# Performance work log

Hardware: AMD Instinct MI355X
Metric: run time of the kernel (lower is better)

The kernel has to match this reference:

```python
import jax, jax.numpy as jnp
import numpy as np

TOPK = 12
D = 256
SCALE = D ** -0.5


def setup_inputs() -> dict:
    key = jax.random.key(0)
    ks = jax.random.split(key, 6)
    N, D_in = 12288, 1024
    def w(k, shape, fan_in):
        return jax.random.normal(k, shape, jnp.float32) / np.float32(np.sqrt(fan_in))
    return {
        "x_path": jax.random.normal(ks[0], (N, D_in), jnp.float32),
        "wsi_w": w(ks[1], (D_in, D), D_in),
        "wsi_b": jnp.zeros((D,), jnp.float32),
        "wh_w": w(ks[2], (D, D), D),
        "wh_b": jnp.zeros((D,), jnp.float32),
        "wt_w": w(ks[3], (D, D), D),
        "wt_b": jnp.zeros((D,), jnp.float32),
        "w1_w": w(ks[4], (D, D), D),
        "w1_b": jnp.zeros((D,), jnp.float32),
        "w2_w": w(ks[5], (D, D), D),
        "w2_b": jnp.zeros((D,), jnp.float32),
    }


def reference(x_path, wsi_w, wsi_b, wh_w, wh_b, wt_w, wt_b, w1_w, w1_b, w2_w, w2_b):
    # wsi_net: Linear(1024,256) + ReLU (dropout is identity in eval)
    h = jax.nn.relu(x_path @ wsi_w + wsi_b)          # [N, D]
    e_h = h @ wh_w + wh_b                            # [N, D]
    e_t = h @ wt_w + wt_b                            # [N, D]
    # dense scaled similarity: [N, N]
    attn_logit = (e_h * SCALE) @ e_t.T
    topk_weight, topk_index = jax.lax.top_k(attn_logit, TOPK)  # [N, K]
    topk_prob = jax.nn.softmax(topk_weight, axis=-1)           # [N, K]
    # gather top-k neighbor tail embeddings
    Nb_h = e_t[topk_index]                           # [N, K, D]
    # eh_r = p * Nb_h + (1-p) (x) e_h   (outer product == broadcast mul)
    eh_r = topk_prob[..., None] * Nb_h + (1.0 - topk_prob)[..., None] * e_h[:, None, :]
    gate = jnp.tanh(e_h[:, None, :] + eh_r)          # [N, K, D]
    ka_weight = jnp.einsum('nkd,nkd->nk', Nb_h, gate)  # [N, K]
    ka_prob = jax.nn.softmax(ka_weight, axis=-1)       # [N, K]
    e_Nh = jnp.einsum('nk,nkd->nd', ka_prob, Nb_h)     # [N, D]
    sum_embedding = jax.nn.relu((e_h + e_Nh) @ w1_w + w1_b)
    bi_embedding = jax.nn.relu((e_h * e_Nh) @ w2_w + w2_b)
    return sum_embedding + bi_embedding              # [N, D]
```

## Files before the change

kernel.cpp:

```cpp
#include <hip/hip_runtime.h>
#include <hip/hip_bf16.h>
#include <cmath>

#define TK 12
#define NROW 12288
#define NEG_BIG (-3.0e38f)
#define MFMA16(a,b,c) __builtin_amdgcn_mfma_f32_16x16x32_f16(a,b,c,0,0,0)

#define NCH 8
#define CTILES 96
#define NPH 48
#define NGRP_TOT 384
#define CAP 256

typedef _Float16 f16x8 __attribute__((ext_vector_type(8)));
typedef _Float16 f16x4 __attribute__((ext_vector_type(4)));
typedef float    f32x4 __attribute__((ext_vector_type(4)));

typedef __attribute__((address_space(1))) const void gvoid_t;
typedef __attribute__((address_space(3))) void lvoid_t;
__device__ __forceinline__ void gload_lds16(const void* g, void* l) {
    __builtin_amdgcn_global_load_lds((gvoid_t*)g, (lvoid_t*)l, 16, 0, 0);
}

__global__ __launch_bounds__(256) void wpack(
    const float* __restrict__ W, _Float16* __restrict__ hi,
    _Float16* __restrict__ lo, int N, int nkt)
{
    const int tid = blockIdx.x * 256 + threadIdx.x;
    const int l = tid & 63;
    const int s = (tid >> 6) % nkt;
    const int cg = tid / (nkt * 64);
    const int krow = s * 32 + 8 * (l >> 4);
    const int col = cg * 16 + (l & 15);
    f16x8 H, L;
    #pragma unroll
    for (int j = 0; j < 8; ++j) {
        float w = W[(size_t)(krow + j) * N + col];
        _Float16 h = (_Float16)w;
        H[j] = h;
        L[j] = (_Float16)(w - (float)h);
    }
    *(f16x8*)(hi + (size_t)tid * 8) = H;
    *(f16x8*)(lo + (size_t)tid * 8) = L;
}

__global__ __launch_bounds__(256) void wpack4(
    const float* __restrict__ W0, const float* __restrict__ W1,
    const float* __restrict__ W2, const float* __restrict__ W3,
    _Float16* __restrict__ base)
{
    const int m = blockIdx.y;
    const float* W = (m == 0) ? W0 : (m == 1) ? W1 : (m == 2) ? W2 : W3;
    _Float16* hi = base + (size_t)m * 131072;
    _Float16* lo = hi + 65536;
    const int tid = blockIdx.x * 256 + threadIdx.x;
    const int l = tid & 63;
    const int s = (tid >> 6) & 7;
    const int cg = tid >> 9;
    const int krow = s * 32 + 8 * (l >> 4);
    const int col = cg * 16 + (l & 15);
    f16x8 H, L;
    #pragma unroll
    for (int j = 0; j < 8; ++j) {
        float w = W[(size_t)(krow + j) * 256 + col];
        _Float16 h = (_Float16)w;
        H[j] = h;
        L[j] = (_Float16)(w - (float)h);
    }
    *(f16x8*)(hi + (size_t)tid * 8) = H;
    *(f16x8*)(lo + (size_t)tid * 8) = L;
}

template<bool RELU>
__global__ __launch_bounds__(256) void gemm_mfma(
    const float* __restrict__ A1,
    const _Float16* __restrict__ Wh, const _Float16* __restrict__ Wl,
    const float* __restrict__ bias, float* __restrict__ C, int K)
{
    __shared__ _Float16 aH[2048], aL[2048];
    __shared__ _Float16 wH[2048], wL[2048];
    const int tid = threadIdx.x, lane = tid & 63, wave = tid >> 6;
    const int rb = blockIdx.y * 64;
    const int cbg = blockIdx.x * 4;
    const int nkt = K >> 5;

    const int arow = rb + wave * 16 + (lane & 15);
    const int acol0 = 8 * (lane >> 4);
    const float* a1p = A1 + (size_t)arow * K + acol0;
    const size_t wbase = ((size_t)(cbg + wave) * nkt) * 512 + lane * 8;

    f32x4 acc[4];
    #pragma unroll
    for (int rg = 0; rg < 4; ++rg) acc[rg] = (f32x4){0.f,0.f,0.f,0.f};

    float4 pa0 = *(const float4*)(a1p);
    float4 pa1 = *(const float4*)(a1p + 4);
    f16x8 pwh = *(const f16x8*)(Wh + wbase);
    f16x8 pwl = *(const f16x8*)(Wl + wbase);

    for (int kt = 0; kt < nkt; ++kt) {
        __syncthreads();
        {
            float v[8] = {pa0.x, pa0.y, pa0.z, pa0.w, pa1.x, pa1.y, pa1.z, pa1.w};
            f16x8 H, L;
            #pragma unroll
            for (int j = 0; j < 8; ++j) {
                _Float16 h = (_Float16)v[j];
                H[j] = h;
                L[j] = (_Float16)(v[j] - (float)h);
            }
            *(f16x8*)&aH[tid*8] = H;
            *(f16x8*)&aL[tid*8] = L;
            *(f16x8*)&wH[tid*8] = pwh;
            *(f16x8*)&wL[tid*8] = pwl;
        }
        __syncthreads();
        if (kt + 1 < nkt) {
            pa0 = *(const float4*)(a1p + (kt+1)*32);
            pa1 = *(const float4*)(a1p + (kt+1)*32 + 4);
            pwh = *(const f16x8*)(Wh + wbase + (size_t)(kt+1)*512);
            pwl = *(const f16x8*)(Wl + wbase + (size_t)(kt+1)*512);
        }
        f16x8 wh = *(const f16x8*)&wH[(wave*64 + lane)*8];
        f16x8 wl = *(const f16x8*)&wL[(wave*64 + lane)*8];
        #pragma unroll
        for (int rg = 0; rg < 4; ++rg) {
            f16x8 ah = *(const f16x8*)&aH[(rg*64 + lane)*8];
            f16x8 al = *(const f16x8*)&aL[(rg*64 + lane)*8];
            acc[rg] = MFMA16(wh, ah, acc[rg]);
            acc[rg] = MFMA16(wl, ah, acc[rg]);
            acc[rg] = MFMA16(wh, al, acc[rg]);
        }
    }
    const int col = (cbg + wave)*16 + 4*(lane >> 4);
    float4 b4 = *(const float4*)(bias + col);
    #pragma unroll
    for (int rg = 0; rg < 4; ++rg) {
        const int row = rb + rg*16 + (lane & 15);
        float4 o;
        o.x = acc[rg][0] + b4.x; o.y = acc[rg][1] + b4.y;
        o.z = acc[rg][2] + b4.z; o.w = acc[rg][3] + b4.w;
        if (RELU) {
            o.x = fmaxf(o.x, 0.f); o.y = fmaxf(o.y, 0.f);
            o.z = fmaxf(o.z, 0.f); o.w = fmaxf(o.w, 0.f);
        }
        *(float4*)(C + (size_t)row*256 + col) = o;
    }
}

template<int DMODE>
__global__ __launch_bounds__(256) void gemm_dual(
    const float* __restrict__ A1, const float* __restrict__ A2,
    const _Float16* __restrict__ W1h, const _Float16* __restrict__ W1l,
    const _Float16* __restrict__ W2h, const _Float16* __restrict__ W2l,
    const float* __restrict__ bias1, const float* __restrict__ bias2,
    float* __restrict__ C1, float* __restrict__ C2,
    _Float16* __restrict__ P1, _Float16* __restrict__ P2)
{
    __shared__ _Float16 aH[2][2048], aL[2][2048];
    __shared__ _Float16 wH[2][2048], wL[2][2048];
    const int tid = threadIdx.x, lane = tid & 63, wave = tid >> 6;
    const int rb = blockIdx.y * 64;
    const int cbg = blockIdx.x * 4;

    const int arow = rb + wave * 16 + (lane & 15);
    const int acol0 = 8 * (lane >> 4);
    const float* a1p = A1 + (size_t)arow * 256 + acol0;
    const float* a2p = (DMODE == 1) ? (A2 + (size_t)arow * 256 + acol0) : nullptr;
    const size_t wbase = ((size_t)(cbg + wave) * 8) * 512 + lane * 8;

    f32x4 acc1[4], acc2[4];
    #pragma unroll
    for (int rg = 0; rg < 4; ++rg) {
        acc1[rg] = (f32x4){0.f,0.f,0.f,0.f};
        acc2[rg] = (f32x4){0.f,0.f,0.f,0.f};
    }

    float4 pa0 = *(const float4*)(a1p);
    float4 pa1 = *(const float4*)(a1p + 4);
    float4 pb0, pb1;
    if (DMODE == 1) { pb0 = *(const float4*)(a2p); pb1 = *(const float4*)(a2p + 4); }
    f16x8 pw1h = *(const f16x8*)(W1h + wbase);
    f16x8 pw1l = *(const f16x8*)(W1l + wbase);
    f16x8 pw2h = *(const f16x8*)(W2h + wbase);
    f16x8 pw2l = *(const f16x8*)(W2l + wbase);

    for (int kt = 0; kt < 8; ++kt) {
        __syncthreads();
        {
            float v[8] = {pa0.x, pa0.y, pa0.z, pa0.w, pa1.x, pa1.y, pa1.z, pa1.w};
            if (DMODE == 0) {
                f16x8 H, L;
                #pragma unroll
                for (int j = 0; j < 8; ++j) {
                    _Float16 h = (_Float16)v[j];
                    H[j] = h;
                    L[j] = (_Float16)(v[j] - (float)h);
                }
                *(f16x8*)&aH[0][tid*8] = H;
                *(f16x8*)&aL[0][tid*8] = L;
            } else {
                float b[8] = {pb0.x, pb0.y, pb0.z, pb0.w, pb1.x, pb1.y, pb1.z, pb1.w};
                f16x8 Hs, Ls, Hm, Lm;
                #pragma unroll
                for (int j = 0; j < 8; ++j) {
                    float s = v[j] + b[j];
                    float m = v[j] * b[j];
                    _Float16 hs = (_Float16)s;
                    _Float16 hm = (_Float16)m;
                    Hs[j] = hs; Ls[j] = (_Float16)(s - (float)hs);
                    Hm[j] = hm; Lm[j] = (_Float16)(m - (float)hm);
                }
                *(f16x8*)&aH[0][tid*8] = Hs;
                *(f16x8*)&aL[0][tid*8] = Ls;
                *(f16x8*)&aH[1][tid*8] = Hm;
                *(f16x8*)&aL[1][tid*8] = Lm;
            }
            *(f16x8*)&wH[0][tid*8] = pw1h;
            *(f16x8*)&wL[0][tid*8] = pw1l;
            *(f16x8*)&wH[1][tid*8] = pw2h;
            *(f16x8*)&wL[1][tid*8] = pw2l;
        }
        __syncthreads();
        if (kt + 1 < 8) {
            pa0 = *(const float4*)(a1p + (kt+1)*32);
            pa1 = *(const float4*)(a1p + (kt+1)*32 + 4);
            if (DMODE == 1) {
                pb0 = *(const float4*)(a2p + (kt+1)*32);
                pb1 = *(const float4*)(a2p + (kt+1)*32 + 4);
            }
            pw1h = *(const f16x8*)(W1h + wbase + (size_t)(kt+1)*512);
            pw1l = *(const f16x8*)(W1l + wbase + (size_t)(kt+1)*512);
            pw2h = *(const f16x8*)(W2h + wbase + (size_t)(kt+1)*512);
            pw2l = *(const f16x8*)(W2l + wbase + (size_t)(kt+1)*512);
        }
        f16x8 w1h = *(const f16x8*)&wH[0][(wave*64 + lane)*8];
        f16x8 w1l = *(const f16x8*)&wL[0][(wave*64 + lane)*8];
        f16x8 w2h = *(const f16x8*)&wH[1][(wave*64 + lane)*8];
        f16x8 w2l = *(const f16x8*)&wL[1][(wave*64 + lane)*8];
        #pragma unroll
        for (int rg = 0; rg < 4; ++rg) {
            f16x8 ah0 = *(const f16x8*)&aH[0][(rg*64 + lane)*8];
            f16x8 al0 = *(const f16x8*)&aL[0][(rg*64 + lane)*8];
            acc1[rg] = MFMA16(w1h, ah0, acc1[rg]);
            acc1[rg] = MFMA16(w1l, ah0, acc1[rg]);
            acc1[rg] = MFMA16(w1h, al0, acc1[rg]);
            f16x8 ah1 = (DMODE == 1) ? *(const f16x8*)&aH[1][(rg*64 + lane)*8] : ah0;
            f16x8 al1 = (DMODE == 1) ? *(const f16x8*)&aL[1][(rg*64 + lane)*8] : al0;
            acc2[rg] = MFMA16(w2h, ah1, acc2[rg]);
            acc2[rg] = MFMA16(w2l, ah1, acc2[rg]);
            acc2[rg] = MFMA16(w2h, al1, acc2[rg]);
        }
    }
    const int col = (cbg + wave)*16 + 4*(lane >> 4);
    float4 b14 = *(const float4*)(bias1 + col);
    float4 b24 = *(const float4*)(bias2 + col);
    #pragma unroll
    for (int rg = 0; rg < 4; ++rg) {
        const int row = rb + rg*16 + (lane & 15);
        if (DMODE == 0) {
            float4 o1, o2;
            o1.x = acc1[rg][0] + b14.x; o1.y = acc1[rg][1] + b14.y;
            o1.z = acc1[rg][2] + b14.z; o1.w = acc1[rg][3] + b14.w;
            o2.x = acc2[rg][0] + b24.x; o2.y = acc2[rg][1] + b24.y;
            o2.z = acc2[rg][2] + b24.z; o2.w = acc2[rg][3] + b24.w;
            *(float4*)(C1 + (size_t)row*256 + col) = o1;
            *(float4*)(C2 + (size_t)row*256 + col) = o2;
            const size_t poff = ((size_t)(row >> 4)*8 + (col >> 5))*512
                              + (((col & 31) >> 3)*16 + (row & 15))*8 + (col & 7);
            f16x4 p1, p2;
            p1[0] = (_Float16)(o1.x * 0.0625f); p1[1] = (_Float16)(o1.y * 0.0625f);
            p1[2] = (_Float16)(o1.z * 0.0625f); p1[3] = (_Float16)(o1.w * 0.0625f);
            p2[0] = (_Float16)o2.x; p2[1] = (_Float16)o2.y;
            p2[2] = (_Float16)o2.z; p2[3] = (_Float16)o2.w;
            *(f16x4*)(P1 + poff) = p1;
            *(f16x4*)(P2 + poff) = p2;
        } else {
            float4 o;
            o.x = fmaxf(acc1[rg][0] + b14.x, 0.f) + fmaxf(acc2[rg][0] + b24.x, 0.f);
            o.y = fmaxf(acc1[rg][1] + b14.y, 0.f) + fmaxf(acc2[rg][1] + b24.y, 0.f);
            o.z = fmaxf(acc1[rg][2] + b14.z, 0.f) + fmaxf(acc2[rg][2] + b24.z, 0.f);
            o.w = fmaxf(acc1[rg][3] + b14.w, 0.f) + fmaxf(acc2[rg][3] + b24.w, 0.f);
            *(float4*)(C1 + (size_t)row*256 + col) = o;
        }
    }
}

__global__ __launch_bounds__(256, 2) void s1_gmax(
    const _Float16* __restrict__ ehh, const _Float16* __restrict__ eth,
    unsigned* __restrict__ g32, unsigned char* __restrict__ gcol)
{
    __shared__ _Float16 abuf[3][8192];
    const int tid = threadIdx.x, lane = tid & 63, wave = tid >> 6;
    const int chunk = blockIdx.x & (NCH-1);
    const int rblk = blockIdx.x >> 3;
    const int rg0 = rblk * 8 + wave * 2;

    f16x8 bh[2][8];
    #pragma unroll
    for (int rs = 0; rs < 2; ++rs) {
        const _Float16* p = ehh + (size_t)(rg0 + rs)*4096 + lane*8;
        #pragma unroll
        for (int s = 0; s < 8; ++s) bh[rs][s] = *(const f16x8*)(p + s*512);
    }
    #pragma unroll
    for (int rs = 0; rs < 2; ++rs)
        #pragma unroll
        for (int s = 0; s < 8; ++s)
            asm volatile("" : "+v"(bh[rs][s]));

    const int rsw = (lane >> 4) & 1;
    const int myrow = (rg0 + rsw)*16 + (lane & 15);
    const size_t rowbase = (size_t)myrow*NGRP_TOT + chunk*NPH;

    const _Float16* gsrc = eth + (size_t)chunk * CTILES * 4096;
    #pragma unroll
    for (int ph = 0; ph < 2; ++ph) {
        #pragma unroll
        for (int i = 0; i < 4; ++i) {
            const int u = wave*4 + i;
            gload_lds16(gsrc + (size_t)(ph*2 + (u>>3))*4096 + (u&7)*512 + lane*8,
                        &abuf[ph][u*512]);
        }
    }
    asm volatile("s_waitcnt vmcnt(4) lgkmcnt(0)" ::: "memory");
    __builtin_amdgcn_s_barrier();
    asm volatile("" ::: "memory");

    int cur = 0;
    for (int pp = 0; pp < 6; ++pp) {
        unsigned resv[8];
        unsigned long long colv = 0;
        #pragma unroll
        for (int q = 0; q < 8; ++q) {
            const int p = pp*8 + q;
            int nx = cur + 2; if (nx >= 3) nx -= 3;
            if (p + 2 < NPH) {
                #pragma unroll
                for (int i = 0; i < 4; ++i) {
                    const int u = wave*4 + i;
                    gload_lds16(gsrc + (size_t)((p+2)*2 + (u>>3))*4096 + (u&7)*512 + lane*8,
                                &abuf[nx][u*512]);
                }
            }
            float m1a = NEG_BIG, m2a = NEG_BIG; int mca = 0;
            float m1b = NEG_BIG, m2b = NEG_BIG; int mcb = 0;
            __builtin_amdgcn_s_setprio(1);
            #pragma unroll
            for (int tt = 0; tt < 2; ++tt) {
                f32x4 aE[2], aO[2];
                #pragma unroll
                for (int rs = 0; rs < 2; ++rs) {
                    aE[rs] = (f32x4){0.f,0.f,0.f,0.f};
                    aO[rs] = (f32x4){0.f,0.f,0.f,0.f};
                }
                #pragma unroll
                for (int s = 0; s < 8; ++s) {
                    f16x8 ah = *(const f16x8*)&abuf[cur][tt*4096 + s*512 + lane*8];
                    if (s & 1) {
                        aO[0] = MFMA16(ah, bh[0][s], aO[0]);
                        aO[1] = MFMA16(ah, bh[1][s], aO[1]);
                    } else {
                        aE[0] = MFMA16(ah, bh[0][s], aE[0]);
                        aE[1] = MFMA16(ah, bh[1][s], aE[1]);
                    }
                }
                f32x4 a0 = aE[0] + aO[0];
                f32x4 a1 = aE[1] + aO[1];
                const int cb = tt*16 + 4*(lane >> 4);
                #pragma unroll
                for (int e = 0; e < 4; ++e) {
                    bool g0 = a0[e] > m1a;
                    m2a = fmaxf(m2a, g0 ? m1a : a0[e]);
                    mca = g0 ? (cb + e) : mca;
                    m1a = fmaxf(m1a, a0[e]);
                    bool g1 = a1[e] > m1b;
                    m2b = fmaxf(m2b, g1 ? m1b : a1[e]);
                    mcb = g1 ? (cb + e) : mcb;
                    m1b = fmaxf(m1b, a1[e]);
                }
            }
            __builtin_amdgcn_s_setprio(0);
            #pragma unroll
            for (int k = 16; k <= 32; k <<= 1) {
                float o1 = __shfl_xor(m1a, k); int oc = __shfl_xor(mca, k);
                float o2 = __shfl_xor(m2a, k);
                bool gt = o1 > m1a;
                m2a = fmaxf(fmaxf(m2a, o2), gt ? m1a : o1);
                mca = gt ? oc : mca;
                m1a = fmaxf(m1a, o1);
                float p1 = __shfl_xor(m1b, k); int pc = __shfl_xor(mcb, k);
                float p2 = __shfl_xor(m2b, k);
                bool ht = p1 > m1b;
                m2b = fmaxf(fmaxf(m2b, p2), ht ? m1b : p1);
                mcb = ht ? pc : mcb;
                m1b = fmaxf(m1b, p1);
            }
            {
                float M1 = rsw ? m1b : m1a;
                float M2 = rsw ? m2b : m2a;
                int   MC = rsw ? mcb : mca;
                unsigned short h1 = __builtin_bit_cast(unsigned short, (_Float16)M1);
                unsigned short h2 = __builtin_bit_cast(unsigned short, (_Float16)M2);
                resv[q] = ((unsigned)h1 << 16) | h2;
                colv |= (unsigned long long)(unsigned char)MC << (8*q);
            }
            if (q == 7 && lane < 32) {
                const size_t base = rowbase + pp*8;
                uint4 v0; v0.x = resv[0]; v0.y = resv[1]; v0.z = resv[2]; v0.w = resv[3];
                uint4 v1; v1.x = resv[4]; v1.y = resv[5]; v1.z = resv[6]; v1.w = resv[7];
                *(uint4*)(g32 + base)     = v0;
                *(uint4*)(g32 + base + 4) = v1;
                *(unsigned long long*)(gcol + base) = colv;
            }
            if (p + 2 < NPH) {
                if (q == 7) { asm volatile("s_waitcnt vmcnt(7)" ::: "memory"); }
                else        { asm volatile("s_waitcnt vmcnt(4)" ::: "memory"); }
            } else {
                asm volatile("s_waitcnt vmcnt(0)" ::: "memory");
            }
            __builtin_amdgcn_s_barrier();
            asm volatile("" ::: "memory");
            cur = cur + 1; if (cur >= 3) cur = 0;
        }
    }
    asm volatile("s_waitcnt vmcnt(0)" ::: "memory");
}

__global__ __launch_bounds__(256) void b2_emit(
    const unsigned* __restrict__ g32, const unsigned char* __restrict__ gcol,
    unsigned* __restrict__ cnt, int* __restrict__ cand)
{
    const int lane = threadIdx.x & 63;
    const int wave = threadIdx.x >> 6;
    const int row  = blockIdx.x * 4 + wave;

    const unsigned* gr = g32 + (size_t)row*NGRP_TOT + lane*6;
    uint2 u0 = *(const uint2*)gr;
    uint2 u1 = *(const uint2*)(gr + 2);
    uint2 u2 = *(const uint2*)(gr + 4);
    unsigned uu[6] = {u0.x, u0.y, u1.x, u1.y, u2.x, u2.y};
    float m1[6], m2[6];
    #pragma unroll
    for (int i = 0; i < 6; ++i) {
        m1[i] = (float)__builtin_bit_cast(_Float16, (unsigned short)(uu[i] >> 16));
        m2[i] = (float)__builtin_bit_cast(_Float16, (unsigned short)(uu[i] & 0xffffu));
    }

    float sl[6];
    #pragma unroll
    for (int j = 0; j < 6; ++j) sl[j] = NEG_BIG;
    #pragma unroll
    for (int i = 0; i < 6; ++i) {
        float v = m1[i];
        #pragma unroll
        for (int j = 5; j >= 1; --j)
            sl[j] = __builtin_amdgcn_fmed3f(v, sl[j], sl[j-1]);
        sl[0] = fmaxf(v, sl[0]);
    }

    int hi = 0;
    float t12 = NEG_BIG;
    #pragma unroll 1
    for (int o = 0; o < TK; ++o) {
        float head = (hi < 6) ? sl[hi] : NEG_BIG;
        float bv = head; int bl = lane;
        #pragma unroll
        for (int off = 1; off <= 32; off <<= 1) {
            float ov = __shfl_xor(bv, off);
            int   ol = __shfl_xor(bl, off);
            bool take = (ov > bv) || (ov == bv && ol < bl);
            bv = take ? ov : bv;
            bl = take ? ol : bl;
        }
        if (lane == bl) hi++;
        t12 = bv;
    }
    const float tau = t12 - 0.02f;

    int n = 0;
    int* crow = cand + (size_t)row * CAP;
    #pragma unroll 1
    for (int i = 0; i < 6; ++i) {
        const bool hit1 = m1[i] >= tau;
        const bool expn = hit1 && (m2[i] >= tau);
        const bool single = hit1 && !expn;
        unsigned long long ms = __ballot(single);
        if (single) {
            const int pos = n + __popcll(ms & ((1ull << lane) - 1ull));
            if (pos < CAP) {
                const int g = lane*6 + i;
                crow[pos] = g*32 + (int)gcol[(size_t)row*NGRP_TOT + g];
            }
        }
        n += __popcll(ms);
        unsigned long long me = __ballot(expn);
        while (me) {
            const int src = __builtin_ctzll(me);
            me &= me - 1ull;
            const int cb = (src*6 + i) * 32;
            if (lane < 32) {
                const int pos = n + lane;
                if (pos < CAP) crow[pos] = cb + lane;
            }
            n += 32;
        }
    }
    if (lane == 0) cnt[row] = (unsigned)((n < CAP) ? n : CAP);
}

__global__ __launch_bounds__(256) void s3_tail(
    const float* __restrict__ e_h, const float* __restrict__ e_t,
    const unsigned int* __restrict__ cnt, const int* __restrict__ cand,
    float* __restrict__ e_Nh)
{
    __shared__ float sbuf[4][64];
    const int lane = threadIdx.x & 63;
    const int wave = threadIdx.x >> 6;
    const int row  = blockIdx.x * 4 + wave;
    const int quad = lane & 3;
    const int cg   = lane >> 2;

    const int cn = (int)min(cnt[row], (unsigned)CAP);
    const float* ehr = e_h + (size_t)row * 256;

    float4 ehv[16];
    #pragma unroll
    for (int j = 0; j < 16; ++j)
        ehv[j] = *(const float4*)(ehr + j*16 + quad*4);

    float v[4]; int c[4];
    #pragma unroll
    for (int i = 0; i < 4; ++i) {
        const int idx = lane + 64*i;
        c[i] = (idx < cn) ? cand[(size_t)row*CAP + idx] : (0x7ffffff0 + i);
        v[i] = NEG_BIG;
    }

    #pragma unroll 1
    for (int ch = 0; ch < 4; ++ch) {
        if (cn <= 64*ch) break;
        #pragma unroll
        for (int b = 0; b < 4; ++b) {
            const int ci = ch*64 + b*16 + cg;
            const bool act = ci < cn;
            const int col = act ? cand[(size_t)row*CAP + ci] : 0;
            const float* etr = e_t + (size_t)col * 256;
            float s = 0.f;
            #pragma unroll
            for (int j = 0; j < 16; ++j) {
                float4 bb = *(const float4*)(etr + j*16 + quad*4);
                s += ehv[j].x*bb.x + ehv[j].y*bb.y + ehv[j].z*bb.z + ehv[j].w*bb.w;
            }
            s += __shfl_xor(s, 1);
            s += __shfl_xor(s, 2);
            if (quad == 0) sbuf[wave][b*16 + cg] = s;
        }
        const int idx = ch*64 + lane;
        float sv = sbuf[wave][lane];
        if (idx < cn) v[ch] = sv * 0.0625f;
    }

    float tvv[TK]; int ti[TK];
    #pragma unroll
    for (int o = 0; o < TK; ++o) {
        float bv = v[0]; int bc = c[0];
        #pragma unroll
        for (int i = 1; i < 4; ++i) {
            bool take = (v[i] > bv) || (v[i] == bv && c[i] < bc);
            bv = take ? v[i] : bv;
            bc = take ? c[i] : bc;
        }
        #pragma unroll
        for (int off = 32; off; off >>= 1) {
            float ov = __shfl_xor(bv, off);
            int   oc = __shfl_xor(bc, off);
            bool take = (ov > bv) || (ov == bv && oc < bc);
            bv = take ? ov : bv;
            bc = take ? oc : bc;
        }
        tvv[o] = bv; ti[o] = bc;
        #pragma unroll
        for (int i = 0; i < 4; ++i)
            if (c[i] == bc) v[i] = NEG_BIG;
    }

    float p[TK]; float Z = 0.f;
    #pragma unroll
    for (int j = 0; j < TK; ++j) { p[j] = expf(tvv[j] - tvv[0]); Z += p[j]; }
    const float invZ = 1.f / Z;
    #pragma unroll
    for (int j = 0; j < TK; ++j) p[j] *= invZ;

    float4 eh = *(const float4*)(ehr + lane * 4);

    float4 nb[TK]; float kw[TK];
    #pragma unroll
    for (int k = 0; k < TK; ++k) {
        float4 n = *(const float4*)(e_t + (size_t)ti[k] * 256 + lane * 4);
        nb[k] = n;
        const float pk = p[k], qk = 1.f - p[k];
        float4 gt;
        gt.x = tanhf(eh.x + (pk * n.x + qk * eh.x));
        gt.y = tanhf(eh.y + (pk * n.y + qk * eh.y));
        gt.z = tanhf(eh.z + (pk * n.z + qk * eh.z));
        gt.w = tanhf(eh.w + (pk * n.w + qk * eh.w));
        float d = n.x*gt.x + n.y*gt.y + n.z*gt.z + n.w*gt.w;
        #pragma unroll
        for (int off = 32; off; off >>= 1) d += __shfl_xor(d, off);
        kw[k] = d;
    }

    float km = kw[0];
    #pragma unroll
    for (int k = 1; k < TK; ++k) km = fmaxf(km, kw[k]);
    float kz = 0.f; float kp[TK];
    #pragma unroll
    for (int k = 0; k < TK; ++k) { kp[k] = expf(kw[k] - km); kz += kp[k]; }
    const float invKZ = 1.f / kz;

    float4 acc = make_float4(0.f, 0.f, 0.f, 0.f);
    #pragma unroll
    for (int k = 0; k < TK; ++k) {
        acc.x += kp[k] * nb[k].x;
        acc.y += kp[k] * nb[k].y;
        acc.z += kp[k] * nb[k].z;
        acc.w += kp[k] * nb[k].w;
    }
    acc.x *= invKZ; acc.y *= invKZ; acc.z *= invKZ; acc.w *= invKZ;
    *(float4*)(e_Nh + (size_t)row * 256 + lane * 4) = acc;
}

extern "C" void kernel_launch(void* const* d_in, const int* in_sizes, int n_in,
                              void* d_out, int out_size, void* d_ws, size_t ws_size,
                              hipStream_t stream)
{
    (void)in_sizes; (void)n_in; (void)out_size; (void)ws_size;
    const float* x     = (const float*)d_in[0];
    const float* wsi_w = (const float*)d_in[1];
    const float* wsi_b = (const float*)d_in[2];
    const float* wh_w  = (const float*)d_in[3];
    const float* wh_b  = (const float*)d_in[4];
    const float* wt_w  = (const float*)d_in[5];
    const float* wt_b  = (const float*)d_in[6];
    const float* w1_w  = (const float*)d_in[7];
    const float* w1_b  = (const float*)d_in[8];
    const float* w2_w  = (const float*)d_in[9];
    const float* w2_b  = (const float*)d_in[10];
    float* out = (float*)d_out;
    float* ws  = (float*)d_ws;

    const int M = NROW;
    const size_t ND = (size_t)M * 256;

    float* h    = ws;
    float* e_h  = ws + ND;
    float* e_t  = ws + 2*ND;
    _Float16* ehh = (_Float16*)(ws + 3*ND);
    _Float16* eth = (_Float16*)(ws + 3*ND + ND/2);
    size_t o = 4*ND;
    unsigned* g32 = (unsigned*)(ws + o);          o += (size_t)NGRP_TOT*NROW;
    unsigned char* gcol = (unsigned char*)(ws + o); o += (size_t)NGRP_TOT*NROW/4;
    unsigned int* cnt = (unsigned int*)(ws + o);  o += NROW;
    int* cand = (int*)(ws + o);                   o += (size_t)NROW*CAP;
    _Float16* hp = (_Float16*)(ws + o);
    _Float16* wsiH = hp;
    _Float16* wsiL = hp + 262144;
    _Float16* w4base = hp + 524288;
    _Float16* whH  = w4base;
    _Float16* whL  = w4base + 65536;
    _Float16* wtH  = w4base + 2*65536;
    _Float16* wtL  = w4base + 3*65536;
    _Float16* w1H  = w4base + 4*65536;
    _Float16* w1L  = w4base + 5*65536;
    _Float16* w2H  = w4base + 6*65536;
    _Float16* w2L  = w4base + 7*65536;
    float* e_Nh = h;

    wpack<<<128, 256, 0, stream>>>(wsi_w, wsiH, wsiL, 256, 32);
    wpack4<<<dim3(32, 4), 256, 0, stream>>>(wh_w, wt_w, w1_w, w2_w, w4base);

    gemm_mfma<true><<<dim3(4, M/64), 256, 0, stream>>>(
        x, wsiH, wsiL, wsi_b, h, 1024);
    gemm_dual<0><<<dim3(4, M/64), 256, 0, stream>>>(
        h, nullptr, whH, whL, wtH, wtL, wh_b, wt_b, e_h, e_t, ehh, eth);
    s1_gmax<<<NCH*96, 256, 0, stream>>>(ehh, eth, g32, gcol);
    b2_emit<<<M/4, 256, 0, stream>>>(g32, gcol, cnt, cand);
    s3_tail<<<M/4, 256, 0, stream>>>(e_h, e_t, cnt, cand, e_Nh);
    gemm_dual<1><<<dim3(4, M/64), 256, 0, stream>>>(
        e_h, e_Nh, w1H, w1L, w2H, w2L, w1_b, w2_b, out, nullptr, nullptr, nullptr);
}
```

Before: 343.8 us.

## Track top-3 per column group to cut full-group candidate expansion; use fast tanh/exp

The similarity pre-pass now keeps the top three values and two column indices per 32-column group instead of top two and one index. The emit stage can then add up to two exact candidates per group and only expands the whole group when the third value passes the threshold. This is meant to shrink the candidate lists and the rescoring work in the tail kernel, at the price of more compare/select work and twice the per-group summary traffic. Separately, the tail kernel swaps tanhf/expf/division for fast approximate intrinsics, which slightly reduces accuracy.

```diff
diff --git a/kernel.cpp b/kernel.cpp
--- a/kernel.cpp
+++ b/kernel.cpp
@@ -21,6 +21,11 @@
 typedef __attribute__((address_space(3))) void lvoid_t;
 __device__ __forceinline__ void gload_lds16(const void* g, void* l) {
     __builtin_amdgcn_global_load_lds((gvoid_t*)g, (lvoid_t*)l, 16, 0, 0);
+}
+
+__device__ __forceinline__ float ftanh(float x) {
+    float e = __expf(2.f * x);
+    return 1.f - __fdividef(2.f, e + 1.f);
 }
 
 __global__ __launch_bounds__(256) void wpack(
@@ -287,9 +292,17 @@
     }
 }
 
+#define INS3(v, c, M1, C1v, M2, C2v, M3)                 \
+    { bool g1 = (v) > M1, g2 = (v) > M2, g3 = (v) > M3;  \
+      M3 = g2 ? M2 : (g3 ? (v) : M3);                    \
+      M2 = g1 ? M1 : (g2 ? (v) : M2);                    \
+      C2v = g1 ? C1v : (g2 ? (c) : C2v);                 \
+      M1 = g1 ? (v) : M1;                                \
+      C1v = g1 ? (c) : C1v; }
+
 __global__ __launch_bounds__(256, 2) void s1_gmax(
     const _Float16* __restrict__ ehh, const _Float16* __restrict__ eth,
-    unsigned* __restrict__ g32, unsigned char* __restrict__ gcol)
+    uint2* __restrict__ g64)
 {
     __shared__ _Float16 abuf[3][8192];
     const int tid = threadIdx.x, lane = tid & 63, wave = tid >> 6;
@@ -330,8 +343,7 @@
 
     int cur = 0;
     for (int pp = 0; pp < 6; ++pp) {
-        unsigned resv[8];
-        unsigned long long colv = 0;
+        unsigned resx[8], resy[8];
         #pragma unroll
         for (int q = 0; q < 8; ++q) {
             const int p = pp*8 + q;
@@ -344,8 +356,8 @@
                                 &abuf[nx][u*512]);
                 }
             }
-            float m1a = NEG_BIG, m2a = NEG_BIG; int mca = 0;
-            float m1b = NEG_BIG, m2b = NEG_BIG; int mcb = 0;
+            float m1a = NEG_BIG, m2a = NEG_BIG, m3a = NEG_BIG; int c1a = 0, c2a = 0;
+            float m1b = NEG_BIG, m2b = NEG_BIG, m3b = NEG_BIG; int c1b = 0, c2b = 0;
             __builtin_amdgcn_s_setprio(1);
             #pragma unroll
             for (int tt = 0; tt < 2; ++tt) {
@@ -371,51 +383,51 @@
                 const int cb = tt*16 + 4*(lane >> 4);
                 #pragma unroll
                 for (int e = 0; e < 4; ++e) {
-                    bool g0 = a0[e] > m1a;
-                    m2a = fmaxf(m2a, g0 ? m1a : a0[e]);
-                    mca = g0 ? (cb + e) : mca;
-                    m1a = fmaxf(m1a, a0[e]);
-                    bool g1 = a1[e] > m1b;
-                    m2b = fmaxf(m2b, g1 ? m1b : a1[e]);
-                    mcb = g1 ? (cb + e) : mcb;
-                    m1b = fmaxf(m1b, a1[e]);
+                    INS3(a0[e], cb + e, m1a, c1a, m2a, c2a, m3a);
+                    INS3(a1[e], cb + e, m1b, c1b, m2b, c2b, m3b);
                 }
             }
             __builtin_amdgcn_s_setprio(0);
             #pragma unroll
             for (int k = 16; k <= 32; k <<= 1) {
-                float o1 = __shfl_xor(m1a, k); int oc = __shfl_xor(mca, k);
-                float o2 = __shfl_xor(m2a, k);
-                bool gt = o1 > m1a;
-                m2a = fmaxf(fmaxf(m2a, o2), gt ? m1a : o1);
-                mca = gt ? oc : mca;
-                m1a = fmaxf(m1a, o1);
-                float p1 = __shfl_xor(m1b, k); int pc = __shfl_xor(mcb, k);
-                float p2 = __shfl_xor(m2b, k);
-                bool ht = p1 > m1b;
-                m2b = fmaxf(fmaxf(m2b, p2), ht ? m1b : p1);
-                mcb = ht ? pc : mcb;
-                m1b = fmaxf(m1b, p1);
+                float o1 = __shfl_xor(m1a, k); int oc1 = __shfl_xor(c1a, k);
+                float o2 = __shfl_xor(m2a, k); int oc2 = __shfl_xor(c2a, k);
+                float o3 = __shfl_xor(m3a, k);
+                INS3(o1, oc1, m1a, c1a, m2a, c2a, m3a);
+                INS3(o2, oc2, m1a, c1a, m2a, c2a, m3a);
+                m3a = fmaxf(m3a, o3);
+                float p1 = __shfl_xor(m1b, k); int pc1 = __shfl_xor(c1b, k);
+                float p2 = __shfl_xor(m2b, k); int pc2 = __shfl_xor(c2b, k);
+                float p3 = __shfl_xor(m3b, k);
+                INS3(p1, pc1, m1b, c1b, m2b, c2b, m3b);
+                INS3(p2, pc2, m1b, c1b, m2b, c2b, m3b);
+                m3b = fmaxf(m3b, p3);
             }
             {
                 float M1 = rsw ? m1b : m1a;
                 float M2 = rsw ? m2b : m2a;
-                int   MC = rsw ? mcb : mca;
+                float M3 = rsw ? m3b : m3a;
+                int   C1v = rsw ? c1b : c1a;
+                int   C2v = rsw ? c2b : c2a;
                 unsigned short h1 = __builtin_bit_cast(unsigned short, (_Float16)M1);
                 unsigned short h2 = __builtin_bit_cast(unsigned short, (_Float16)M2);
-                resv[q] = ((unsigned)h1 << 16) | h2;
-                colv |= (unsigned long long)(unsigned char)MC << (8*q);
+                unsigned short h3 = __builtin_bit_cast(unsigned short, (_Float16)M3);
+                resx[q] = ((unsigned)h1 << 16) | h2;
+                resy[q] = ((unsigned)h3 << 16) | ((unsigned)(C1v & 0xff) << 8) | (unsigned)(C2v & 0xff);
             }
             if (q == 7 && lane < 32) {
-                const size_t base = rowbase + pp*8;
-                uint4 v0; v0.x = resv[0]; v0.y = resv[1]; v0.z = resv[2]; v0.w = resv[3];
-                uint4 v1; v1.x = resv[4]; v1.y = resv[5]; v1.z = resv[6]; v1.w = resv[7];
-                *(uint4*)(g32 + base)     = v0;
-                *(uint4*)(g32 + base + 4) = v1;
-                *(unsigned long long*)(gcol + base) = colv;
+                uint2* base = g64 + rowbase + pp*8;
+                uint4 v0; v0.x = resx[0]; v0.y = resy[0]; v0.z = resx[1]; v0.w = resy[1];
+                uint4 v1; v1.x = resx[2]; v1.y = resy[2]; v1.z = resx[3]; v1.w = resy[3];
+                uint4 v2; v2.x = resx[4]; v2.y = resy[4]; v2.z = resx[5]; v2.w = resy[5];
+                uint4 v3; v3.x = resx[6]; v3.y = resy[6]; v3.z = resx[7]; v3.w = resy[7];
+                *(uint4*)(base)     = v0;
+                *(uint4*)(base + 2) = v1;
+                *(uint4*)(base + 4) = v2;
+                *(uint4*)(base + 6) = v3;
             }
             if (p + 2 < NPH) {
-                if (q == 7) { asm volatile("s_waitcnt vmcnt(7)" ::: "memory"); }
+                if (q == 7) { asm volatile("s_waitcnt vmcnt(8)" ::: "memory"); }
                 else        { asm volatile("s_waitcnt vmcnt(4)" ::: "memory"); }
             } else {
                 asm volatile("s_waitcnt vmcnt(0)" ::: "memory");
@@ -429,23 +441,25 @@
 }
 
 __global__ __launch_bounds__(256) void b2_emit(
-    const unsigned* __restrict__ g32, const unsigned char* __restrict__ gcol,
+    const uint2* __restrict__ g64,
     unsigned* __restrict__ cnt, int* __restrict__ cand)
 {
     const int lane = threadIdx.x & 63;
     const int wave = threadIdx.x >> 6;
     const int row  = blockIdx.x * 4 + wave;
 
-    const unsigned* gr = g32 + (size_t)row*NGRP_TOT + lane*6;
-    uint2 u0 = *(const uint2*)gr;
-    uint2 u1 = *(const uint2*)(gr + 2);
-    uint2 u2 = *(const uint2*)(gr + 4);
-    unsigned uu[6] = {u0.x, u0.y, u1.x, u1.y, u2.x, u2.y};
-    float m1[6], m2[6];
+    const uint2* gr = g64 + (size_t)row*NGRP_TOT + lane*6;
+    uint4 q0 = *(const uint4*)gr;
+    uint4 q1 = *(const uint4*)(gr + 2);
+    uint4 q2 = *(const uint4*)(gr + 4);
+    unsigned gx[6] = {q0.x, q0.z, q1.x, q1.z, q2.x, q2.z};
+    unsigned gy[6] = {q0.y, q0.w, q1.y, q1.w, q2.y, q2.w};
+    float m1[6], m2[6], m3[6];
     #pragma unroll
     for (int i = 0; i < 6; ++i) {
-        m1[i] = (float)__builtin_bit_cast(_Float16, (unsigned short)(uu[i] >> 16));
-        m2[i] = (float)__builtin_bit_cast(_Float16, (unsigned short)(uu[i] & 0xffffu));
+        m1[i] = (float)__builtin_bit_cast(_Float16, (unsigned short)(gx[i] >> 16));
+        m2[i] = (float)__builtin_bit_cast(_Float16, (unsigned short)(gx[i] & 0xffffu));
+        m3[i] = (float)__builtin_bit_cast(_Float16, (unsigned short)(gy[i] >> 16));
     }
 
     float sl[6];
@@ -483,19 +497,23 @@
     int* crow = cand + (size_t)row * CAP;
     #pragma unroll 1
     for (int i = 0; i < 6; ++i) {
-        const bool hit1 = m1[i] >= tau;
-        const bool expn = hit1 && (m2[i] >= tau);
-        const bool single = hit1 && !expn;
-        unsigned long long ms = __ballot(single);
-        if (single) {
-            const int pos = n + __popcll(ms & ((1ull << lane) - 1ull));
-            if (pos < CAP) {
-                const int g = lane*6 + i;
-                crow[pos] = g*32 + (int)gcol[(size_t)row*NGRP_TOT + g];
-            }
-        }
-        n += __popcll(ms);
-        unsigned long long me = __ballot(expn);
+        const bool exp3 = m3[i] >= tau;
+        const bool e1 = (m1[i] >= tau) && !exp3;
+        const bool e2 = (m2[i] >= tau) && !exp3;
+        const int g = lane*6 + i;
+        unsigned long long ms1 = __ballot(e1);
+        if (e1) {
+            const int pos = n + __popcll(ms1 & ((1ull << lane) - 1ull));
+            if (pos < CAP) crow[pos] = g*32 + (int)((gy[i] >> 8) & 0xffu);
+        }
+        n += __popcll(ms1);
+        unsigned long long ms2 = __ballot(e2);
+        if (e2) {
+            const int pos = n + __popcll(ms2 & ((1ull << lane) - 1ull));
+            if (pos < CAP) crow[pos] = g*32 + (int)(gy[i] & 0xffu);
+        }
+        n += __popcll(ms2);
+        unsigned long long me = __ballot(exp3);
         while (me) {
             const int src = __builtin_ctzll(me);
             me &= me - 1ull;
@@ -588,8 +606,8 @@
 
     float p[TK]; float Z = 0.f;
     #pragma unroll
-    for (int j = 0; j < TK; ++j) { p[j] = expf(tvv[j] - tvv[0]); Z += p[j]; }
-    const float invZ = 1.f / Z;
+    for (int j = 0; j < TK; ++j) { p[j] = __expf(tvv[j] - tvv[0]); Z += p[j]; }
+    const float invZ = __fdividef(1.f, Z);
     #pragma unroll
     for (int j = 0; j < TK; ++j) p[j] *= invZ;
 
@@ -602,10 +620,10 @@
         nb[k] = n;
         const float pk = p[k], qk = 1.f - p[k];
         float4 gt;
-        gt.x = tanhf(eh.x + (pk * n.x + qk * eh.x));
-        gt.y = tanhf(eh.y + (pk * n.y + qk * eh.y));
-        gt.z = tanhf(eh.z + (pk * n.z + qk * eh.z));
-        gt.w = tanhf(eh.w + (pk * n.w + qk * eh.w));
+        gt.x = ftanh(eh.x + (pk * n.x + qk * eh.x));
+        gt.y = ftanh(eh.y + (pk * n.y + qk * eh.y));
+        gt.z = ftanh(eh.z + (pk * n.z + qk * eh.z));
+        gt.w = ftanh(eh.w + (pk * n.w + qk * eh.w));
         float d = n.x*gt.x + n.y*gt.y + n.z*gt.z + n.w*gt.w;
         #pragma unroll
         for (int off = 32; off; off >>= 1) d += __shfl_xor(d, off);
@@ -617,8 +635,8 @@
     for (int k = 1; k < TK; ++k) km = fmaxf(km, kw[k]);
     float kz = 0.f; float kp[TK];
     #pragma unroll
-    for (int k = 0; k < TK; ++k) { kp[k] = expf(kw[k] - km); kz += kp[k]; }
-    const float invKZ = 1.f / kz;
+    for (int k = 0; k < TK; ++k) { kp[k] = __expf(kw[k] - km); kz += kp[k]; }
+    const float invKZ = __fdividef(1.f, kz);
 
     float4 acc = make_float4(0.f, 0.f, 0.f, 0.f);
     #pragma unroll
@@ -660,8 +678,7 @@
     _Float16* ehh = (_Float16*)(ws + 3*ND);
     _Float16* eth = (_Float16*)(ws + 3*ND + ND/2);
     size_t o = 4*ND;
-    unsigned* g32 = (unsigned*)(ws + o);          o += (size_t)NGRP_TOT*NROW;
-    unsigned char* gcol = (unsigned char*)(ws + o); o += (size_t)NGRP_TOT*NROW/4;
+    uint2* g64 = (uint2*)(ws + o);                o += (size_t)NGRP_TOT*NROW*2;
     unsigned int* cnt = (unsigned int*)(ws + o);  o += NROW;
     int* cand = (int*)(ws + o);                   o += (size_t)NROW*CAP;
     _Float16* hp = (_Float16*)(ws + o);
@@ -685,8 +702,8 @@
         x, wsiH, wsiL, wsi_b, h, 1024);
     gemm_dual<0><<<dim3(4, M/64), 256, 0, stream>>>(
         h, nullptr, whH, whL, wtH, wtL, wh_b, wt_b, e_h, e_t, ehh, eth);
-    s1_gmax<<<NCH*96, 256, 0, stream>>>(ehh, eth, g32, gcol);
-    b2_emit<<<M/4, 256, 0, stream>>>(g32, gcol, cnt, cand);
+    s1_gmax<<<NCH*96, 256, 0, stream>>>(ehh, eth, g64);
+    b2_emit<<<M/4, 256, 0, stream>>>(g64, cnt, cand);
     s3_tail<<<M/4, 256, 0, stream>>>(e_h, e_t, cnt, cand, e_Nh);
     gemm_dual<1><<<dim3(4, M/64), 256, 0, stream>>>(
         e_h, e_Nh, w1H, w1L, w2H, w2L, w1_b, w2_b, out, nullptr, nullptr, nullptr);
```

Result: no change. 349.3 us (+1.6%).
